# Optimization experiments

Hardware: AMD Instinct MI355X
Metric: run time of the kernel (lower is better)

Reference implementation:

```python
import jax, jax.numpy as jnp
import numpy as np
from jax.scipy.special import gammaln

BIG_NEG = -1e9
MAX_K = 20  # args.sm_max_span_length


def setup_inputs() -> dict:
    key = jax.random.key(0)
    ks = jax.random.split(key, 7)
    B, N, d, C = 16, 2048, 256, 128
    features = jax.random.normal(ks[0], (B, N, d), dtype=jnp.float32)
    lengths = jax.random.randint(ks[1], (B,), N // 2, N + 1)
    gaussian_means = jax.random.normal(ks[2], (C, d), dtype=jnp.float32)
    cov_diag = jax.random.uniform(ks[3], (d,), minval=0.5, maxval=1.5, dtype=jnp.float32)
    transition_logits = jax.random.normal(ks[4], (C, C), dtype=jnp.float32)
    init_logits = jax.random.uniform(ks[5], (C,), dtype=jnp.float32)
    poisson_log_rates = jax.random.normal(ks[6], (C,), dtype=jnp.float32) * 0.5 + 1.5
    return {"features": features, "lengths": lengths, "gaussian_means": gaussian_means,
            "cov_diag": cov_diag, "transition_logits": transition_logits,
            "init_logits": init_logits, "poisson_log_rates": poisson_log_rates}


def _emission_log_probs(features, means, cov_diag):
    # Diagonal-covariance MultivariateNormal log-prob, one class per column.
    # Quadratic form expanded to avoid materializing [B,N,C,d].
    inv_var = 1.0 / cov_diag
    d = features.shape[-1]
    const = -0.5 * (d * jnp.log(2.0 * jnp.pi) + jnp.sum(jnp.log(cov_diag)))
    xq = jnp.einsum('bnd,d->bn', features * features, inv_var)          # [B,N]
    mq = jnp.einsum('cd,d->c', means * means, inv_var)                  # [C]
    xm = jnp.einsum('bnd,cd->bnc', features, means * inv_var)           # [B,N,C]
    return const - 0.5 * (xq[..., None] + mq[None, None, :] - 2.0 * xm)  # [B,N,C]


def _length_log_probs(log_rates, K):
    # Poisson log-prob for span lengths k = 1..K.
    ks = jnp.arange(1, K + 1, dtype=jnp.float32)[:, None]               # [K,1]
    return ks * log_rates[None, :] - jnp.exp(log_rates)[None, :] - gammaln(ks + 1.0)  # [K,C]


def _transition_log_probs(transition_logits):
    C = transition_logits.shape[0]
    masked = jnp.where(jnp.eye(C, dtype=bool), BIG_NEG, transition_logits)  # no self-transitions
    return jax.nn.log_softmax(masked, axis=0)  # normalized over destination class (dim 0)


def _semimarkov_logZ(emis_lp, lengths, init_lp, trans_lp, len_lp, K):
    # Segmental (semi-Markov) CRF forward algorithm with sliding-window span sums.
    B, N, C = emis_lp.shape
    cum = jnp.concatenate([jnp.zeros((B, 1, C), emis_lp.dtype), jnp.cumsum(emis_lp, axis=1)], axis=1)
    cum_pad = jnp.concatenate([jnp.zeros((B, K, C), emis_lp.dtype), cum], axis=1)  # idx t+K <-> position t
    beta0 = jnp.full((B, N + 1 + K, C), BIG_NEG, emis_lp.dtype)
    beta0 = beta0.at[:, K, :].set(init_lp[None, :])  # position 0: initial distribution
    len_rev = len_lp[::-1]  # len_rev[j] == length log-prob of span length K-j

    def step(beta, t):
        w = jax.lax.dynamic_slice(beta, (0, t, 0), (B, K, C))        # beta at positions t-K..t-1
        cw = jax.lax.dynamic_slice(cum_pad, (0, t, 0), (B, K, C))
        ct = jax.lax.dynamic_slice(cum_pad, (0, t + K, 0), (B, 1, C))
        span = w + len_rev[None, :, :] + (ct - cw)                    # [B,K,C] span scores ending at t
        alpha_t = jax.nn.logsumexp(span, axis=1)                      # [B,C]
        beta_t = jax.nn.logsumexp(alpha_t[:, None, :] + trans_lp[None, :, :], axis=2)  # to-class
        beta = jax.lax.dynamic_update_slice(beta, beta_t[:, None, :], (0, t + K, 0))
        return beta, alpha_t

    _, alphas = jax.lax.scan(step, beta0, jnp.arange(1, N + 1))       # alphas: [N,B,C]
    final = alphas[lengths - 1, jnp.arange(B)]                        # [B,C] at each sequence end
    return jax.nn.logsumexp(final, axis=1)                            # [B] log partition


def reference(features, lengths, gaussian_means, cov_diag, transition_logits, init_logits, poisson_log_rates):
    emis_lp = _emission_log_probs(features, gaussian_means, cov_diag)
    init_lp = jax.nn.log_softmax(init_logits, axis=0)
    trans_lp = _transition_log_probs(transition_logits)
    len_lp = _length_log_probs(poisson_log_rates, MAX_K)
    return _semimarkov_logZ(emis_lp, lengths, init_lp, trans_lp, len_lp, MAX_K)
```

## Files before the change

### kernel.cpp

```cpp
#include <hip/hip_runtime.h>
#include <math.h>

#define Bb 16
#define Nn 2048
#define Dd 256
#define Cc 128
#define Kk 20
#define BIG_NEG -1.0e9f

#define WS_EMIS   0
#define WS_MSC    (WS_EMIS + Bb*Nn*Cc)
#define WS_XQ     (WS_MSC + Cc*Dd)
#define WS_ECHAN  (WS_XQ + Bb*Nn)
#define WS_T      (WS_ECHAN + Cc)
#define WS_LEN    (WS_T + Cc*Cc)
#define WS_INIT   (WS_LEN + Kk*Cc)
#define WS_IVAR   (WS_INIT + Cc)

typedef __attribute__((ext_vector_type(8))) short short8;
typedef __attribute__((ext_vector_type(4))) float float4v;
typedef __attribute__((ext_vector_type(2))) float float2v;

__device__ __forceinline__ unsigned short f32_to_bf16(float x) {
  unsigned int u = __builtin_bit_cast(unsigned int, x);
  u = (u + 0x7FFFu + ((u >> 16) & 1u)) >> 16;
  return (unsigned short)u;
}

#define DPP_STEP(x, op, ctrl, rmask)                                          \
  do {                                                                        \
    int _yi = __builtin_amdgcn_update_dpp(                                    \
        __builtin_bit_cast(int, x), __builtin_bit_cast(int, x), ctrl, rmask,  \
        0xF, true);                                                           \
    x = op(x, __builtin_bit_cast(float, _yi));                                \
  } while (0)

__device__ __forceinline__ float dpp_add(float a, float b) { return a + b; }

__device__ __forceinline__ float wave_max64(float x) {
  DPP_STEP(x, fmaxf, 0xB1, 0xF);
  DPP_STEP(x, fmaxf, 0x4E, 0xF);
  DPP_STEP(x, fmaxf, 0x141, 0xF);
  DPP_STEP(x, fmaxf, 0x140, 0xF);
  DPP_STEP(x, fmaxf, 0x142, 0xA);
  DPP_STEP(x, fmaxf, 0x143, 0xC);
  return __builtin_bit_cast(float,
      __builtin_amdgcn_readlane(__builtin_bit_cast(int, x), 63));
}

__device__ __forceinline__ float wave_sum64(float x) {
  DPP_STEP(x, dpp_add, 0xB1, 0xF);
  DPP_STEP(x, dpp_add, 0x4E, 0xF);
  DPP_STEP(x, dpp_add, 0x141, 0xF);
  DPP_STEP(x, dpp_add, 0x140, 0xF);
  DPP_STEP(x, dpp_add, 0x142, 0xA);
  DPP_STEP(x, dpp_add, 0x143, 0xC);
  return __builtin_bit_cast(float,
      __builtin_amdgcn_readlane(__builtin_bit_cast(int, x), 63));
}

__global__ void prep_kernel(const float* __restrict__ means,
                            const float* __restrict__ cov,
                            const float* __restrict__ tl,
                            const float* __restrict__ il,
                            const float* __restrict__ plr,
                            float* __restrict__ ws) {
  __shared__ float s_iv[Dd];
  __shared__ float s_red[4];
  __shared__ float s_tlse[Cc];
  int tid = threadIdx.x;

  float cv = cov[tid];
  float iv = 1.0f / cv;
  s_iv[tid] = iv;
  ws[WS_IVAR + tid] = iv;
  float lg = __logf(cv);
  #pragma unroll
  for (int off = 1; off < 64; off <<= 1) lg += __shfl_xor(lg, off, 64);
  if ((tid & 63) == 0) s_red[tid >> 6] = lg;
  __syncthreads();
  float logdet = s_red[0] + s_red[1] + s_red[2] + s_red[3];
  float cconst = -0.5f * ((float)Dd * 1.8378770664093453f + logdet);

  unsigned short* mscb = (unsigned short*)(ws + WS_MSC);
  for (int idx = tid; idx < Cc * Dd; idx += 256) {
    int d = idx & (Dd - 1);
    mscb[idx] = f32_to_bf16(means[idx] * s_iv[d]);
  }
  if (tid < Cc) {
    float acc = 0.0f;
    for (int d = 0; d < Dd; d++) {
      float m = means[tid * Dd + d];
      acc = fmaf(m * m, s_iv[d], acc);
    }
    ws[WS_ECHAN + tid] = cconst - 0.5f * acc;
  }
  for (int idx = tid; idx < Kk * Cc; idx += 256) {
    int L = idx / Cc + 1;
    int c = idx & (Cc - 1);
    float r = plr[c];
    ws[WS_LEN + idx] = (float)L * r - __expf(r) - lgammaf((float)(L + 1));
  }

  __syncthreads();
  float x = (tid < Cc) ? il[tid] : -INFINITY;
  float mx = x;
  #pragma unroll
  for (int off = 1; off < 64; off <<= 1) mx = fmaxf(mx, __shfl_xor(mx, off, 64));
  if ((tid & 63) == 0) s_red[tid >> 6] = mx;
  __syncthreads();
  float M = fmaxf(s_red[0], s_red[1]);
  float se = (tid < Cc) ? __expf(x - M) : 0.0f;
  #pragma unroll
  for (int off = 1; off < 64; off <<= 1) se += __shfl_xor(se, off, 64);
  __syncthreads();
  if ((tid & 63) == 0) s_red[tid >> 6] = se;
  __syncthreads();
  float lse = M + __logf(s_red[0] + s_red[1]);
  if (tid < Cc) ws[WS_INIT + tid] = x - lse;

  if (tid < Cc) {
    int j = tid;
    float m2 = -INFINITY;
    for (int i = 0; i < Cc; i++) if (i != j) m2 = fmaxf(m2, tl[i * Cc + j]);
    float s2 = 0.0f;
    for (int i = 0; i < Cc; i++) if (i != j) s2 += __expf(tl[i * Cc + j] - m2);
    s_tlse[j] = m2 + __logf(s2);
  }
  __syncthreads();
  for (int idx = tid; idx < Cc * Cc; idx += 256) {
    int i = idx / Cc;
    int j = idx & (Cc - 1);
    ws[WS_T + idx] = (i == j) ? 0.0f : __expf(tl[idx] - s_tlse[j]);
  }
}

__global__ void xq_kernel(const float* __restrict__ f, float* __restrict__ ws) {
  int pos = blockIdx.x * 4 + (threadIdx.x >> 6);
  int lane = threadIdx.x & 63;
  const float4 fv = *(const float4*)&f[(size_t)pos * Dd + lane * 4];
  const float4 vv = *(const float4*)&ws[WS_IVAR + lane * 4];
  float a = fv.x * fv.x * vv.x + fv.y * fv.y * vv.y +
            fv.z * fv.z * vv.z + fv.w * fv.w * vv.w;
  #pragma unroll
  for (int off = 1; off < 64; off <<= 1) a += __shfl_xor(a, off, 64);
  if (lane == 0) ws[WS_XQ + pos] = a;
}

__launch_bounds__(256)
__global__ void emis_mfma_kernel(const float* __restrict__ f, float* __restrict__ ws) {
  const unsigned short* msc = (const unsigned short*)(ws + WS_MSC);
  float* emis = ws + WS_EMIS;
  int tid = threadIdx.x;
  int w = tid >> 6, lane = tid & 63, g = lane >> 4, l16 = lane & 15;
  int b = blockIdx.x >> 6;
  int n0 = (blockIdx.x & 63) << 5;
  int c0 = w << 5;

  const float* fbase = f + (size_t)(b * Nn + n0) * Dd;
  float4v acc[2][2];
  #pragma unroll
  for (int rt = 0; rt < 2; rt++)
    #pragma unroll
    for (int ct = 0; ct < 2; ct++) acc[rt][ct] = (float4v){0.f, 0.f, 0.f, 0.f};

  #pragma unroll
  for (int k0 = 0; k0 < Dd; k0 += 32) {
    int kk = k0 + g * 8;
    short8 afr[2], bfr[2];
    #pragma unroll
    for (int rt = 0; rt < 2; rt++) {
      const float* src = fbase + (size_t)(rt * 16 + l16) * Dd + kk;
      float4 v0 = *(const float4*)src;
      float4 v1 = *(const float4*)(src + 4);
      short8 fr;
      fr[0] = (short)f32_to_bf16(v0.x); fr[1] = (short)f32_to_bf16(v0.y);
      fr[2] = (short)f32_to_bf16(v0.z); fr[3] = (short)f32_to_bf16(v0.w);
      fr[4] = (short)f32_to_bf16(v1.x); fr[5] = (short)f32_to_bf16(v1.y);
      fr[6] = (short)f32_to_bf16(v1.z); fr[7] = (short)f32_to_bf16(v1.w);
      afr[rt] = fr;
    }
    #pragma unroll
    for (int ct = 0; ct < 2; ct++)
      bfr[ct] = *(const short8*)&msc[(size_t)(c0 + ct * 16 + l16) * Dd + kk];
    #pragma unroll
    for (int rt = 0; rt < 2; rt++)
      #pragma unroll
      for (int ct = 0; ct < 2; ct++)
        acc[rt][ct] = __builtin_amdgcn_mfma_f32_16x16x32_bf16(afr[rt], bfr[ct], acc[rt][ct], 0, 0, 0);
  }

  #pragma unroll
  for (int rt = 0; rt < 2; rt++) {
    #pragma unroll
    for (int ct = 0; ct < 2; ct++) {
      int cc = c0 + ct * 16 + l16;
      float ec = ws[WS_ECHAN + cc];
      #pragma unroll
      for (int r = 0; r < 4; r++) {
        int row = rt * 16 + g * 4 + r;
        int nn = n0 + row;
        emis[(size_t)(b * Nn + nn) * Cc + cc] =
            ec - 0.5f * ws[WS_XQ + b * Nn + nn] + acc[rt][ct][r];
      }
    }
  }
}

__launch_bounds__(64, 1)
__global__ void scan_kernel(const int* __restrict__ lengths,
                            const float* __restrict__ ws,
                            float* __restrict__ out) {
  __shared__ __align__(16) unsigned short p_lds[Cc];

  int lane = threadIdx.x;
  int g = lane >> 4;
  int l15 = lane & 15;
  int c0 = g * 32 + l15;
  int c1 = c0 + 16;
  int b = blockIdx.x;
  int len_b = lengths[b];
  const float* emis = ws + WS_EMIS + (size_t)b * Nn * Cc;

  short8 Tf[8][4];
  {
    const float* T = ws + WS_T;
    #pragma unroll
    for (int nt = 0; nt < 8; nt++)
      #pragma unroll
      for (int kc = 0; kc < 4; kc++) {
        const float* src = &T[(size_t)(nt * 16 + l15) * Cc + kc * 32 + g * 8];
        short8 fr;
        #pragma unroll
        for (int j = 0; j < 8; j++) fr[j] = (short)f32_to_bf16(src[j]);
        Tf[nt][kc] = fr;
      }
  }

  float2v elen[Kk];
  #pragma unroll
  for (int k = 0; k < Kk; k++)
    elen[k] = (float2v){__expf(ws[WS_LEN + k * Cc + c0]),
                        __expf(ws[WS_LEN + k * Cc + c1])};

  float2v E[Kk - 1];
  #pragma unroll
  for (int s = 0; s < Kk - 1; s++) E[s] = (float2v){0.0f, 0.0f};

  float2v q = (float2v){__expf(ws[WS_INIT + c0]), __expf(ws[WS_INIT + c1])};
  float2v Stail = (float2v){0.0f, 0.0f};
  float2v cum = (float2v){0.0f, 0.0f};
  float2v Dlt = (float2v){0.0f, 0.0f};
  float2v dcomp = (float2v){0.0f, 0.0f};

  float2v e[8], en[8];
  float me[8];
  #pragma unroll
  for (int j = 0; j < 8; j++)
    e[j] = (float2v){emis[(size_t)j * Cc + c0], emis[(size_t)j * Cc + c1]};
  #pragma unroll
  for (int j = 0; j < 8; j++) me[j] = wave_max64(fmaxf(e[j].x, e[j].y));
  float2v ee = (float2v){__expf(e[0].x - me[0]), __expf(e[0].y - me[0])};

  bool done = false;
  for (int tg = 1; tg <= Nn && !done; tg += 8) {
    #pragma unroll
    for (int i = 0; i < 8; i++) {
      int t = tg + i;
      float2v ecur = e[i];
      float2v S = q * elen[0] + Stail;

      if (t == len_b) {
        float ax = cum.x + ecur.x + Dlt.x + __logf(fmaxf(S.x, 1e-37f));
        float ay = cum.y + ecur.y + Dlt.y + __logf(fmaxf(S.y, 1e-37f));
        float Mb = wave_max64(fmaxf(ax, ay));
        float ps = wave_sum64(__expf(ax - Mb) + __expf(ay - Mb));
        if (lane == 0) out[b] = Mb + __logf(ps);
        done = true;
        break;
      }

      float2v v = S * ee;
      p_lds[c0] = f32_to_bf16(v.x);
      p_lds[c1] = f32_to_bf16(v.y);
      asm volatile("s_waitcnt lgkmcnt(0)" ::: "memory");
      short8 pa0 = *(const short8*)&p_lds[g * 8];
      short8 pa1 = *(const short8*)&p_lds[32 + g * 8];
      short8 pa2 = *(const short8*)&p_lds[64 + g * 8];
      short8 pa3 = *(const short8*)&p_lds[96 + g * 8];

      float wv = fmaxf(wave_max64(fmaxf(v.x, v.y)), 1.0e-30f);
      float r = __builtin_amdgcn_rcpf(wv);

      if (i == 0) {
        #pragma unroll
        for (int j = 0; j < 8; j++) {
          int rr = tg + 7 + j;
          if (rr > Nn - 1) rr = Nn - 1;
          en[j] = (float2v){emis[(size_t)rr * Cc + c0], emis[(size_t)rr * Cc + c1]};
        }
      }

      float4v z = {0.0f, 0.0f, 0.0f, 0.0f};
      float qv[8];
      #pragma unroll
      for (int nt = 0; nt < 8; nt++) {
        float4v x = __builtin_amdgcn_mfma_f32_16x16x32_bf16(pa1, Tf[nt][1],
                      __builtin_amdgcn_mfma_f32_16x16x32_bf16(pa0, Tf[nt][0], z, 0, 0, 0),
                      0, 0, 0);
        float4v y = __builtin_amdgcn_mfma_f32_16x16x32_bf16(pa3, Tf[nt][3],
                      __builtin_amdgcn_mfma_f32_16x16x32_bf16(pa2, Tf[nt][2], z, 0, 0, 0),
                      0, 0, 0);
        qv[nt] = x[0] + y[0];
      }

      float2v sch = ee * r;
      #pragma unroll
      for (int s = Kk - 2; s >= 1; s--) E[s] = E[s - 1] * sch;
      E[0] = q * sch;

      float2v s0 = E[0] * elen[1];
      float2v s1 = E[1] * elen[2];
      float2v s2 = E[2] * elen[3];
      float2v s3 = E[3] * elen[4];
      s0 = E[4] * elen[5] + s0;   s1 = E[5] * elen[6] + s1;
      s2 = E[6] * elen[7] + s2;   s3 = E[7] * elen[8] + s3;
      s0 = E[8] * elen[9] + s0;   s1 = E[9] * elen[10] + s1;
      s2 = E[10] * elen[11] + s2; s3 = E[11] * elen[12] + s3;
      s0 = E[12] * elen[13] + s0; s1 = E[13] * elen[14] + s1;
      s2 = E[14] * elen[15] + s2; s3 = E[15] * elen[16] + s3;
      s0 = E[16] * elen[17] + s0; s1 = E[17] * elen[18] + s1;
      s2 = E[18] * elen[19] + s2;
      Stail = (s0 + s1) + (s2 + s3);

      float dla = me[i] + __logf(wv);
      float2v dd = (float2v){dla, dla} - ecur;
      float2v yk = dd - dcomp;
      float2v t2 = Dlt + yk;
      dcomp = (t2 - Dlt) - yk;
      Dlt = t2;
      cum += ecur;

      if (i >= 2) me[i - 2] = wave_max64(fmaxf(en[i - 2].x, en[i - 2].y));
      if (i < 7)
        ee = (float2v){__expf(e[i + 1].x - me[i + 1]),
                       __expf(e[i + 1].y - me[i + 1])};

      float q0 = (g & 2) ? ((g & 1) ? qv[6] : qv[4]) : ((g & 1) ? qv[2] : qv[0]);
      float q1 = (g & 2) ? ((g & 1) ? qv[7] : qv[5]) : ((g & 1) ? qv[3] : qv[1]);
      q = (float2v){q0 * r, q1 * r};
    }
    if (!done) {
      me[6] = wave_max64(fmaxf(en[6].x, en[6].y));
      me[7] = wave_max64(fmaxf(en[7].x, en[7].y));
      #pragma unroll
      for (int j = 0; j < 8; j++) e[j] = en[j];
      ee = (float2v){__expf(e[0].x - me[0]), __expf(e[0].y - me[0])};
    }
  }
}

extern "C" void kernel_launch(void* const* d_in, const int* in_sizes, int n_in,
                              void* d_out, int out_size, void* d_ws, size_t ws_size,
                              hipStream_t stream) {
  const float* features = (const float*)d_in[0];
  const int* lengths = (const int*)d_in[1];
  const float* means = (const float*)d_in[2];
  const float* cov = (const float*)d_in[3];
  const float* tl = (const float*)d_in[4];
  const float* il = (const float*)d_in[5];
  const float* plr = (const float*)d_in[6];
  float* out = (float*)d_out;
  float* ws = (float*)d_ws;

  prep_kernel<<<1, 256, 0, stream>>>(means, cov, tl, il, plr, ws);
  xq_kernel<<<(Bb * Nn) / 4, 256, 0, stream>>>(features, ws);
  emis_mfma_kernel<<<Bb * (Nn / 32), 256, 0, stream>>>(features, ws);
  scan_kernel<<<Bb, 64, 0, stream>>>(lengths, ws, out);
}
```

Measured before the change: 1.796 ms.

## Split semi-Markov scan across two waves per batch with LDS exchange

The per-batch forward scan now uses two waves, each owning 64 classes and computing half of the bf16 MFMA transition product. Per-step wave maxima, the shared bf16 p vector and emission maxima are exchanged through double-buffered LDS with a block barrier each timestep. This halves per-wave MFMA and vector work on the serial critical path, at the cost of a __syncthreads and extra LDS traffic every step.

```diff
diff --git a/kernel.cpp b/kernel.cpp
--- a/kernel.cpp
+++ b/kernel.cpp
@@ -19,7 +19,6 @@
 
 typedef __attribute__((ext_vector_type(8))) short short8;
 typedef __attribute__((ext_vector_type(4))) float float4v;
-typedef __attribute__((ext_vector_type(2))) float float2v;
 
 __device__ __forceinline__ unsigned short f32_to_bf16(float x) {
   unsigned int u = __builtin_bit_cast(unsigned int, x);
@@ -207,29 +206,33 @@
   }
 }
 
-__launch_bounds__(64, 1)
+__launch_bounds__(128, 1)
 __global__ void scan_kernel(const int* __restrict__ lengths,
                             const float* __restrict__ ws,
                             float* __restrict__ out) {
-  __shared__ __align__(16) unsigned short p_lds[Cc];
-
-  int lane = threadIdx.x;
+  __shared__ __align__(16) unsigned short p_lds[2][Cc];
+  __shared__ float lds_wv[2][2];
+  __shared__ float lds_men[2][2][8];
+  __shared__ float lds_out[2][2];
+
+  int tid = threadIdx.x;
+  int w = tid >> 6;
+  int lane = tid & 63;
   int g = lane >> 4;
   int l15 = lane & 15;
-  int c0 = g * 32 + l15;
-  int c1 = c0 + 16;
+  int c = w * 64 + lane;
   int b = blockIdx.x;
   int len_b = lengths[b];
   const float* emis = ws + WS_EMIS + (size_t)b * Nn * Cc;
 
-  short8 Tf[8][4];
+  short8 Tf[4][4];
   {
     const float* T = ws + WS_T;
     #pragma unroll
-    for (int nt = 0; nt < 8; nt++)
+    for (int nt = 0; nt < 4; nt++)
       #pragma unroll
       for (int kc = 0; kc < 4; kc++) {
-        const float* src = &T[(size_t)(nt * 16 + l15) * Cc + kc * 32 + g * 8];
+        const float* src = &T[(size_t)((w * 4 + nt) * 16 + l15) * Cc + kc * 32 + g * 8];
         short8 fr;
         #pragma unroll
         for (int j = 0; j < 8; j++) fr[j] = (short)f32_to_bf16(src[j]);
@@ -237,59 +240,70 @@
       }
   }
 
-  float2v elen[Kk];
-  #pragma unroll
-  for (int k = 0; k < Kk; k++)
-    elen[k] = (float2v){__expf(ws[WS_LEN + k * Cc + c0]),
-                        __expf(ws[WS_LEN + k * Cc + c1])};
-
-  float2v E[Kk - 1];
-  #pragma unroll
-  for (int s = 0; s < Kk - 1; s++) E[s] = (float2v){0.0f, 0.0f};
-
-  float2v q = (float2v){__expf(ws[WS_INIT + c0]), __expf(ws[WS_INIT + c1])};
-  float2v Stail = (float2v){0.0f, 0.0f};
-  float2v cum = (float2v){0.0f, 0.0f};
-  float2v Dlt = (float2v){0.0f, 0.0f};
-  float2v dcomp = (float2v){0.0f, 0.0f};
-
-  float2v e[8], en[8];
-  float me[8];
-  #pragma unroll
-  for (int j = 0; j < 8; j++)
-    e[j] = (float2v){emis[(size_t)j * Cc + c0], emis[(size_t)j * Cc + c1]};
-  #pragma unroll
-  for (int j = 0; j < 8; j++) me[j] = wave_max64(fmaxf(e[j].x, e[j].y));
-  float2v ee = (float2v){__expf(e[0].x - me[0]), __expf(e[0].y - me[0])};
+  float elen[Kk];
+  #pragma unroll
+  for (int k = 0; k < Kk; k++) elen[k] = __expf(ws[WS_LEN + k * Cc + c]);
+  float elen0 = elen[0];
+
+  float E[Kk - 1];
+  #pragma unroll
+  for (int s = 0; s < Kk - 1; s++) E[s] = 0.0f;
+
+  float q = __expf(ws[WS_INIT + c]);
+  float Stail = 0.0f;
+  float cum = 0.0f;
+  float Dlt = 0.0f, dcomp = 0.0f;
+
+  float e[8], en[8];
+  #pragma unroll
+  for (int j = 0; j < 8; j++) e[j] = emis[(size_t)j * Cc + c];
+  #pragma unroll
+  for (int j = 0; j < 8; j++) {
+    float m = wave_max64(e[j]);
+    if (lane == 0) lds_men[0][w][j] = m;
+  }
+  __syncthreads();
+  float ee = __expf(e[0] - fmaxf(lds_men[0][0][0], lds_men[0][1][0]));
 
   bool done = false;
   for (int tg = 1; tg <= Nn && !done; tg += 8) {
+    int gp = ((tg - 1) >> 3) & 1;
     #pragma unroll
     for (int i = 0; i < 8; i++) {
       int t = tg + i;
-      float2v ecur = e[i];
-      float2v S = q * elen[0] + Stail;
-
-      if (t == len_b) {
-        float ax = cum.x + ecur.x + Dlt.x + __logf(fmaxf(S.x, 1e-37f));
-        float ay = cum.y + ecur.y + Dlt.y + __logf(fmaxf(S.y, 1e-37f));
-        float Mb = wave_max64(fmaxf(ax, ay));
-        float ps = wave_sum64(__expf(ax - Mb) + __expf(ay - Mb));
-        if (lane == 0) out[b] = Mb + __logf(ps);
+      int buf = t & 1;
+      bool fin = (t == len_b);
+      float ecur = e[i];
+      float S = fmaf(q, elen0, Stail);
+      float a = 0.0f;
+
+      if (fin) {
+        a = (cum + ecur) + Dlt + __logf(fmaxf(S, 1e-37f));
+        float Mw = wave_max64(a);
+        if (lane == 0) lds_out[0][w] = Mw;
+      } else {
+        float v = S * ee;
+        p_lds[buf][c] = f32_to_bf16(v);
+        float wvp = wave_max64(v);
+        if (lane == 0) lds_wv[buf][w] = wvp;
+      }
+      __syncthreads();
+
+      if (fin) {
+        float Mb = fmaxf(lds_out[0][0], lds_out[0][1]);
+        float ps = wave_sum64(__expf(a - Mb));
+        if (lane == 0) lds_out[1][w] = ps;
+        __syncthreads();
+        if (tid == 0) out[b] = Mb + __logf(lds_out[1][0] + lds_out[1][1]);
         done = true;
         break;
       }
 
-      float2v v = S * ee;
-      p_lds[c0] = f32_to_bf16(v.x);
-      p_lds[c1] = f32_to_bf16(v.y);
-      asm volatile("s_waitcnt lgkmcnt(0)" ::: "memory");
-      short8 pa0 = *(const short8*)&p_lds[g * 8];
-      short8 pa1 = *(const short8*)&p_lds[32 + g * 8];
-      short8 pa2 = *(const short8*)&p_lds[64 + g * 8];
-      short8 pa3 = *(const short8*)&p_lds[96 + g * 8];
-
-      float wv = fmaxf(wave_max64(fmaxf(v.x, v.y)), 1.0e-30f);
+      short8 pa0 = *(const short8*)&p_lds[buf][g * 8];
+      short8 pa1 = *(const short8*)&p_lds[buf][32 + g * 8];
+      short8 pa2 = *(const short8*)&p_lds[buf][64 + g * 8];
+      short8 pa3 = *(const short8*)&p_lds[buf][96 + g * 8];
+      float wv = fmaxf(fmaxf(lds_wv[buf][0], lds_wv[buf][1]), 1.0e-30f);
       float r = __builtin_amdgcn_rcpf(wv);
 
       if (i == 0) {
@@ -297,14 +311,14 @@
         for (int j = 0; j < 8; j++) {
           int rr = tg + 7 + j;
           if (rr > Nn - 1) rr = Nn - 1;
-          en[j] = (float2v){emis[(size_t)rr * Cc + c0], emis[(size_t)rr * Cc + c1]};
+          en[j] = emis[(size_t)rr * Cc + c];
         }
       }
 
       float4v z = {0.0f, 0.0f, 0.0f, 0.0f};
-      float qv[8];
-      #pragma unroll
-      for (int nt = 0; nt < 8; nt++) {
+      float qv[4];
+      #pragma unroll
+      for (int nt = 0; nt < 4; nt++) {
         float4v x = __builtin_amdgcn_mfma_f32_16x16x32_bf16(pa1, Tf[nt][1],
                       __builtin_amdgcn_mfma_f32_16x16x32_bf16(pa0, Tf[nt][0], z, 0, 0, 0),
                       0, 0, 0);
@@ -314,48 +328,65 @@
         qv[nt] = x[0] + y[0];
       }
 
-      float2v sch = ee * r;
+      float sch = ee * r;
       #pragma unroll
       for (int s = Kk - 2; s >= 1; s--) E[s] = E[s - 1] * sch;
       E[0] = q * sch;
 
-      float2v s0 = E[0] * elen[1];
-      float2v s1 = E[1] * elen[2];
-      float2v s2 = E[2] * elen[3];
-      float2v s3 = E[3] * elen[4];
-      s0 = E[4] * elen[5] + s0;   s1 = E[5] * elen[6] + s1;
-      s2 = E[6] * elen[7] + s2;   s3 = E[7] * elen[8] + s3;
-      s0 = E[8] * elen[9] + s0;   s1 = E[9] * elen[10] + s1;
-      s2 = E[10] * elen[11] + s2; s3 = E[11] * elen[12] + s3;
-      s0 = E[12] * elen[13] + s0; s1 = E[13] * elen[14] + s1;
-      s2 = E[14] * elen[15] + s2; s3 = E[15] * elen[16] + s3;
-      s0 = E[16] * elen[17] + s0; s1 = E[17] * elen[18] + s1;
-      s2 = E[18] * elen[19] + s2;
+      float s0 = E[0] * elen[1];
+      float s1 = E[1] * elen[2];
+      float s2 = E[2] * elen[3];
+      float s3 = E[3] * elen[4];
+      s0 = fmaf(E[4], elen[5], s0);   s1 = fmaf(E[5], elen[6], s1);
+      s2 = fmaf(E[6], elen[7], s2);   s3 = fmaf(E[7], elen[8], s3);
+      s0 = fmaf(E[8], elen[9], s0);   s1 = fmaf(E[9], elen[10], s1);
+      s2 = fmaf(E[10], elen[11], s2); s3 = fmaf(E[11], elen[12], s3);
+      s0 = fmaf(E[12], elen[13], s0); s1 = fmaf(E[13], elen[14], s1);
+      s2 = fmaf(E[14], elen[15], s2); s3 = fmaf(E[15], elen[16], s3);
+      s0 = fmaf(E[16], elen[17], s0); s1 = fmaf(E[17], elen[18], s1);
+      s2 = fmaf(E[18], elen[19], s2);
       Stail = (s0 + s1) + (s2 + s3);
 
-      float dla = me[i] + __logf(wv);
-      float2v dd = (float2v){dla, dla} - ecur;
-      float2v yk = dd - dcomp;
-      float2v t2 = Dlt + yk;
-      dcomp = (t2 - Dlt) - yk;
-      Dlt = t2;
+      float meC = fmaxf(lds_men[gp][0][i], lds_men[gp][1][i]);
+      float dla = meC + __logf(wv);
+      {
+        float dd = dla - ecur;
+        float yk = dd - dcomp;
+        float t2 = Dlt + yk;
+        dcomp = (t2 - Dlt) - yk;
+        Dlt = t2;
+      }
       cum += ecur;
 
-      if (i >= 2) me[i - 2] = wave_max64(fmaxf(en[i - 2].x, en[i - 2].y));
-      if (i < 7)
-        ee = (float2v){__expf(e[i + 1].x - me[i + 1]),
-                       __expf(e[i + 1].y - me[i + 1])};
-
-      float q0 = (g & 2) ? ((g & 1) ? qv[6] : qv[4]) : ((g & 1) ? qv[2] : qv[0]);
-      float q1 = (g & 2) ? ((g & 1) ? qv[7] : qv[5]) : ((g & 1) ? qv[3] : qv[1]);
-      q = (float2v){q0 * r, q1 * r};
+      if (i >= 2) {
+        float m = wave_max64(en[i - 2]);
+        if (lane == 0) lds_men[gp ^ 1][w][i - 2] = m;
+      }
+      if (i == 6) {
+        float m = wave_max64(en[6]);
+        if (lane == 0) lds_men[gp ^ 1][w][6] = m;
+      }
+      if (i == 7) {
+        float m = wave_max64(en[7]);
+        if (lane == 0) lds_men[gp ^ 1][w][7] = m;
+      }
+
+      if (i < 7) {
+        float meN = fmaxf(lds_men[gp][0][i + 1], lds_men[gp][1][i + 1]);
+        ee = __expf(e[i + 1] - meN);
+      }
+
+      float qs01 = (g & 1) ? qv[1] : qv[0];
+      float qs23 = (g & 1) ? qv[3] : qv[2];
+      float qs = (g & 2) ? qs23 : qs01;
+      q = qs * r;
     }
     if (!done) {
-      me[6] = wave_max64(fmaxf(en[6].x, en[6].y));
-      me[7] = wave_max64(fmaxf(en[7].x, en[7].y));
       #pragma unroll
       for (int j = 0; j < 8; j++) e[j] = en[j];
-      ee = (float2v){__expf(e[0].x - me[0]), __expf(e[0].y - me[0])};
+      int gp = ((tg - 1) >> 3) & 1;
+      float me0 = fmaxf(lds_men[gp ^ 1][0][0], lds_men[gp ^ 1][1][0]);
+      ee = __expf(e[0] - me0);
     }
   }
 }
@@ -376,5 +407,5 @@
   prep_kernel<<<1, 256, 0, stream>>>(means, cov, tl, il, plr, ws);
   xq_kernel<<<(Bb * Nn) / 4, 256, 0, stream>>>(features, ws);
   emis_mfma_kernel<<<Bb * (Nn / 32), 256, 0, stream>>>(features, ws);
-  scan_kernel<<<Bb, 64, 0, stream>>>(lengths, ws, out);
-}
+  scan_kernel<<<Bb, 128, 0, stream>>>(lengths, ws, out);
+}
```

Measured after the change: 1.559 ms. -13.2%, faster.

## Precompute bf16 exp-scaled emissions and renormalize scan once per 8 steps

Applied to the files above, without the earlier changes.

Adds a parallel kernel that turns each emission row into bf16 exp(e - rowmax) values plus a per-row max, so the serial scan no longer does per-step exp, emission max reductions or Kahan compensation. The scan now carries a single scalar log offset and rescales its state only once per 8-step group, using a bf16 integer max over the MFMA input fragments in place of a per-step float wave max. The four MFMAs per tile become independent instead of chained pairs, which shortens the dependency chain on the serial critical path. In exchange it adds an extra kernel pass over the emission buffer, stores emissions in reduced precision, and lets values grow for up to 8 steps between rescales, which could risk overflow or underflow and accuracy loss.

```diff
diff --git a/kernel.cpp b/kernel.cpp
--- a/kernel.cpp
+++ b/kernel.cpp
@@ -20,6 +20,9 @@
 typedef __attribute__((ext_vector_type(8))) short short8;
 typedef __attribute__((ext_vector_type(4))) float float4v;
 typedef __attribute__((ext_vector_type(2))) float float2v;
+typedef __attribute__((ext_vector_type(8))) unsigned short u16x8;
+typedef __attribute__((ext_vector_type(4))) unsigned short u16x4;
+typedef __attribute__((ext_vector_type(2))) unsigned short u16x2;
 
 __device__ __forceinline__ unsigned short f32_to_bf16(float x) {
   unsigned int u = __builtin_bit_cast(unsigned int, x);
@@ -57,6 +60,30 @@
   DPP_STEP(x, dpp_add, 0x143, 0xC);
   return __builtin_bit_cast(float,
       __builtin_amdgcn_readlane(__builtin_bit_cast(int, x), 63));
+}
+
+__device__ __forceinline__ float frag_max_to_f32(short8 a, short8 b, short8 c, short8 d) {
+  u16x8 ua = __builtin_bit_cast(u16x8, a), ub = __builtin_bit_cast(u16x8, b);
+  u16x8 uc = __builtin_bit_cast(u16x8, c), ud = __builtin_bit_cast(u16x8, d);
+  u16x8 m8 = __builtin_elementwise_max(__builtin_elementwise_max(ua, ub),
+                                       __builtin_elementwise_max(uc, ud));
+  u16x4 lo4 = __builtin_shufflevector(m8, m8, 0, 1, 2, 3);
+  u16x4 hi4 = __builtin_shufflevector(m8, m8, 4, 5, 6, 7);
+  u16x4 m4 = __builtin_elementwise_max(lo4, hi4);
+  u16x2 lo2 = __builtin_shufflevector(m4, m4, 0, 1);
+  u16x2 hi2 = __builtin_shufflevector(m4, m4, 2, 3);
+  u16x2 m2 = __builtin_elementwise_max(lo2, hi2);
+  unsigned mm = (unsigned)m2[0];
+  unsigned m1 = (unsigned)m2[1];
+  mm = mm > m1 ? mm : m1;
+  {
+    int y = __builtin_amdgcn_update_dpp((int)mm, (int)mm, 0x142, 0xA, 0xF, true);
+    unsigned uy = (unsigned)y; mm = mm > uy ? mm : uy;
+    y = __builtin_amdgcn_update_dpp((int)mm, (int)mm, 0x143, 0xC, 0xF, true);
+    uy = (unsigned)y; mm = mm > uy ? mm : uy;
+  }
+  unsigned full = (unsigned)__builtin_amdgcn_readlane((int)mm, 63);
+  return __builtin_bit_cast(float, full << 16);
 }
 
 __global__ void prep_kernel(const float* __restrict__ means,
@@ -207,6 +234,21 @@
   }
 }
 
+__global__ void esc_kernel(float* __restrict__ ws) {
+  int row = blockIdx.x * 4 + (threadIdx.x >> 6);
+  int lane = threadIdx.x & 63;
+  int c0 = ((lane >> 4) << 5) + (lane & 15);
+  int c1 = c0 + 16;
+  float* rp = ws + WS_EMIS + (size_t)row * Cc;
+  float e0 = rp[c0];
+  float e1 = rp[c1];
+  float m = wave_max64(fmaxf(e0, e1));
+  unsigned p0 = (unsigned)f32_to_bf16(__expf(e0 - m));
+  unsigned p1 = (unsigned)f32_to_bf16(__expf(e1 - m));
+  ((unsigned*)rp)[lane] = p0 | (p1 << 16);
+  if (lane == 0) ws[WS_XQ + row] = m;
+}
+
 __launch_bounds__(64, 1)
 __global__ void scan_kernel(const int* __restrict__ lengths,
                             const float* __restrict__ ws,
@@ -220,7 +262,8 @@
   int c1 = c0 + 16;
   int b = blockIdx.x;
   int len_b = lengths[b];
-  const float* emis = ws + WS_EMIS + (size_t)b * Nn * Cc;
+  const unsigned* escp = (const unsigned*)(ws + WS_EMIS);
+  const float* mep = ws + WS_XQ + b * Nn;
 
   short8 Tf[8][4];
   {
@@ -249,30 +292,33 @@
 
   float2v q = (float2v){__expf(ws[WS_INIT + c0]), __expf(ws[WS_INIT + c1])};
   float2v Stail = (float2v){0.0f, 0.0f};
-  float2v cum = (float2v){0.0f, 0.0f};
-  float2v Dlt = (float2v){0.0f, 0.0f};
-  float2v dcomp = (float2v){0.0f, 0.0f};
-
-  float2v e[8], en[8];
-  float me[8];
+  float A = 0.0f;
+
+  unsigned ed[8], edn[8];
+  float meL, meLn;
   #pragma unroll
   for (int j = 0; j < 8; j++)
-    e[j] = (float2v){emis[(size_t)j * Cc + c0], emis[(size_t)j * Cc + c1]};
-  #pragma unroll
-  for (int j = 0; j < 8; j++) me[j] = wave_max64(fmaxf(e[j].x, e[j].y));
-  float2v ee = (float2v){__expf(e[0].x - me[0]), __expf(e[0].y - me[0])};
-
+    ed[j] = escp[(size_t)(b * Nn + j) * Cc + lane];
+  meL = (lane < 8) ? mep[lane] : 0.0f;
+
+  short8 pa0, pa1, pa2, pa3;
   bool done = false;
   for (int tg = 1; tg <= Nn && !done; tg += 8) {
     #pragma unroll
     for (int i = 0; i < 8; i++) {
       int t = tg + i;
-      float2v ecur = e[i];
+      unsigned e32 = ed[i];
+      float2v escv = (float2v){
+          __builtin_bit_cast(float, e32 << 16),
+          __builtin_bit_cast(float, e32 & 0xFFFF0000u)};
+      float mei = __builtin_bit_cast(float,
+          __builtin_amdgcn_readlane(__builtin_bit_cast(int, meL), i));
       float2v S = q * elen[0] + Stail;
+      float2v v = S * escv;
 
       if (t == len_b) {
-        float ax = cum.x + ecur.x + Dlt.x + __logf(fmaxf(S.x, 1e-37f));
-        float ay = cum.y + ecur.y + Dlt.y + __logf(fmaxf(S.y, 1e-37f));
+        float ax = A + mei + __logf(fmaxf(v.x, 1e-37f));
+        float ay = A + mei + __logf(fmaxf(v.y, 1e-37f));
         float Mb = wave_max64(fmaxf(ax, ay));
         float ps = wave_sum64(__expf(ax - Mb) + __expf(ay - Mb));
         if (lane == 0) out[b] = Mb + __logf(ps);
@@ -280,44 +326,38 @@
         break;
       }
 
-      float2v v = S * ee;
-      p_lds[c0] = f32_to_bf16(v.x);
-      p_lds[c1] = f32_to_bf16(v.y);
+      p_lds[c0] = (unsigned short)(__builtin_bit_cast(unsigned, v.x) >> 16);
+      p_lds[c1] = (unsigned short)(__builtin_bit_cast(unsigned, v.y) >> 16);
       asm volatile("s_waitcnt lgkmcnt(0)" ::: "memory");
-      short8 pa0 = *(const short8*)&p_lds[g * 8];
-      short8 pa1 = *(const short8*)&p_lds[32 + g * 8];
-      short8 pa2 = *(const short8*)&p_lds[64 + g * 8];
-      short8 pa3 = *(const short8*)&p_lds[96 + g * 8];
-
-      float wv = fmaxf(wave_max64(fmaxf(v.x, v.y)), 1.0e-30f);
-      float r = __builtin_amdgcn_rcpf(wv);
+      pa0 = *(const short8*)&p_lds[g * 8];
+      pa1 = *(const short8*)&p_lds[32 + g * 8];
+      pa2 = *(const short8*)&p_lds[64 + g * 8];
+      pa3 = *(const short8*)&p_lds[96 + g * 8];
 
       if (i == 0) {
         #pragma unroll
         for (int j = 0; j < 8; j++) {
-          int rr = tg + 7 + j;
-          if (rr > Nn - 1) rr = Nn - 1;
-          en[j] = (float2v){emis[(size_t)rr * Cc + c0], emis[(size_t)rr * Cc + c1]};
+          int rr = tg + 7 + j; if (rr > Nn - 1) rr = Nn - 1;
+          edn[j] = escp[(size_t)(b * Nn + rr) * Cc + lane];
         }
+        int rm = tg + 7 + lane; if (rm > Nn - 1) rm = Nn - 1;
+        meLn = (lane < 8) ? mep[rm] : 0.0f;
       }
 
       float4v z = {0.0f, 0.0f, 0.0f, 0.0f};
       float qv[8];
       #pragma unroll
       for (int nt = 0; nt < 8; nt++) {
-        float4v x = __builtin_amdgcn_mfma_f32_16x16x32_bf16(pa1, Tf[nt][1],
-                      __builtin_amdgcn_mfma_f32_16x16x32_bf16(pa0, Tf[nt][0], z, 0, 0, 0),
-                      0, 0, 0);
-        float4v y = __builtin_amdgcn_mfma_f32_16x16x32_bf16(pa3, Tf[nt][3],
-                      __builtin_amdgcn_mfma_f32_16x16x32_bf16(pa2, Tf[nt][2], z, 0, 0, 0),
-                      0, 0, 0);
-        qv[nt] = x[0] + y[0];
+        float4v m0 = __builtin_amdgcn_mfma_f32_16x16x32_bf16(pa0, Tf[nt][0], z, 0, 0, 0);
+        float4v m1 = __builtin_amdgcn_mfma_f32_16x16x32_bf16(pa1, Tf[nt][1], z, 0, 0, 0);
+        float4v m2 = __builtin_amdgcn_mfma_f32_16x16x32_bf16(pa2, Tf[nt][2], z, 0, 0, 0);
+        float4v m3 = __builtin_amdgcn_mfma_f32_16x16x32_bf16(pa3, Tf[nt][3], z, 0, 0, 0);
+        qv[nt] = (m0[0] + m1[0]) + (m2[0] + m3[0]);
       }
 
-      float2v sch = ee * r;
-      #pragma unroll
-      for (int s = Kk - 2; s >= 1; s--) E[s] = E[s - 1] * sch;
-      E[0] = q * sch;
+      #pragma unroll
+      for (int s = Kk - 2; s >= 1; s--) E[s] = E[s - 1] * escv;
+      E[0] = q * escv;
 
       float2v s0 = E[0] * elen[1];
       float2v s1 = E[1] * elen[2];
@@ -333,29 +373,23 @@
       s2 = E[18] * elen[19] + s2;
       Stail = (s0 + s1) + (s2 + s3);
 
-      float dla = me[i] + __logf(wv);
-      float2v dd = (float2v){dla, dla} - ecur;
-      float2v yk = dd - dcomp;
-      float2v t2 = Dlt + yk;
-      dcomp = (t2 - Dlt) - yk;
-      Dlt = t2;
-      cum += ecur;
-
-      if (i >= 2) me[i - 2] = wave_max64(fmaxf(en[i - 2].x, en[i - 2].y));
-      if (i < 7)
-        ee = (float2v){__expf(e[i + 1].x - me[i + 1]),
-                       __expf(e[i + 1].y - me[i + 1])};
+      A += mei;
 
       float q0 = (g & 2) ? ((g & 1) ? qv[6] : qv[4]) : ((g & 1) ? qv[2] : qv[0]);
       float q1 = (g & 2) ? ((g & 1) ? qv[7] : qv[5]) : ((g & 1) ? qv[3] : qv[1]);
-      q = (float2v){q0 * r, q1 * r};
+      q = (float2v){q0, q1};
     }
     if (!done) {
-      me[6] = wave_max64(fmaxf(en[6].x, en[6].y));
-      me[7] = wave_max64(fmaxf(en[7].x, en[7].y));
-      #pragma unroll
-      for (int j = 0; j < 8; j++) e[j] = en[j];
-      ee = (float2v){__expf(e[0].x - me[0]), __expf(e[0].y - me[0])};
+      float wv = fmaxf(frag_max_to_f32(pa0, pa1, pa2, pa3), 1.0e-30f);
+      float r = __builtin_amdgcn_rcpf(wv);
+      q = q * r;
+      Stail = Stail * r;
+      #pragma unroll
+      for (int s = 0; s < Kk - 1; s++) E[s] = E[s] * r;
+      A += __logf(wv);
+      #pragma unroll
+      for (int j = 0; j < 8; j++) ed[j] = edn[j];
+      meL = meLn;
     }
   }
 }
@@ -376,5 +410,6 @@
   prep_kernel<<<1, 256, 0, stream>>>(means, cov, tl, il, plr, ws);
   xq_kernel<<<(Bb * Nn) / 4, 256, 0, stream>>>(features, ws);
   emis_mfma_kernel<<<Bb * (Nn / 32), 256, 0, stream>>>(features, ws);
+  esc_kernel<<<(Bb * Nn) / 4, 256, 0, stream>>>(ws);
   scan_kernel<<<Bb, 64, 0, stream>>>(lengths, ws, out);
 }
```

After: 2.020 ms. 1.12x slower.
